# Performance work log

Hardware: AMD Instinct MI355X
Metric: run time of the kernel (lower is better)

The kernel has to match this reference:

```python
import jax, jax.numpy as jnp
import numpy as np

E, MAX_M, K, N = 8, 2048, 2048, 8192

def setup_inputs() -> dict:
    key = jax.random.key(0)
    k1, k2, k3 = jax.random.split(key, 3)
    x_padded = jax.random.normal(k1, (E, MAX_M, K), dtype=jnp.float32)
    stacked_weights = jax.random.normal(k2, (E, N, K), dtype=jnp.float32) * 0.02
    m_sizes = jax.random.randint(k3, (E,), 0, MAX_M, dtype=jnp.int32)
    return {"x_padded": x_padded, "stacked_weights": stacked_weights, "m_sizes": m_sizes}

def reference(x_padded, stacked_weights, m_sizes):
    # valid-token mask per expert: [E, MAX_M]
    mask = (jnp.arange(MAX_M, dtype=jnp.int32)[None, :] < m_sizes[:, None])
    # zero padded rows (pad_expert_inputs fills with zeros)
    x = jnp.where(mask[:, :, None], x_padded, jnp.zeros((), x_padded.dtype))
    # grouped GEMM via batched matmul: [E, M, K] x [E, N, K]^T -> [E, M, N]
    out = jnp.einsum('emk,enk->emn', x, stacked_weights)
    # rows beyond m_sizes[i] are sliced away in the original; mask them to zero
    return jnp.where(mask[:, :, None], out, jnp.zeros((), out.dtype))
```

## Files before the change

kernel.cpp:

```cpp
#include <hip/hip_runtime.h>
#include <hip/hip_bf16.h>


#define NE   8
#define MAXM 2048
#define KD   2048
#define ND   8192

#define BM   256
#define BN   256
#define BK   64
#define NT   (KD/BK)
#define TMB  (MAXM/BM)
#define TNB  (ND/BN)

typedef __attribute__((ext_vector_type(8))) short          short8;
typedef __attribute__((ext_vector_type(8))) unsigned short us8;
typedef __attribute__((ext_vector_type(4))) float          f32x4;
typedef __attribute__((ext_vector_type(4))) unsigned short us4;

__device__ __forceinline__ unsigned short f2bf(float f) {
    union { float f; unsigned u; } v; v.f = f;
    unsigned u = v.u;
    return (unsigned short)((u + 0x7FFFu + ((u >> 16) & 1u)) >> 16);
}

__device__ __forceinline__ void gload16(const void* g, void* l) {
    __builtin_amdgcn_global_load_lds(
        (const __attribute__((address_space(1))) void*)g,
        (__attribute__((address_space(3))) void*)l, 16, 0, 0);
}

__global__ __launch_bounds__(256) void cvt_kernel(const float* __restrict__ src,
                                                  unsigned short* __restrict__ dst,
                                                  int n8) {
    int i = blockIdx.x * blockDim.x + threadIdx.x;
    int stride = gridDim.x * blockDim.x;
    for (; i < n8; i += stride) {
        const f32x4* s = (const f32x4*)(src + (size_t)i * 8);
        f32x4 a = s[0], b = s[1];
        us8 v = (us8){f2bf(a[0]), f2bf(a[1]), f2bf(a[2]), f2bf(a[3]),
                      f2bf(b[0]), f2bf(b[1]), f2bf(b[2]), f2bf(b[3])};
        *(us8*)(dst + (size_t)i * 8) = v;
    }
}

__global__ __launch_bounds__(512, 2) void ggemm_8ph(
    const unsigned short* __restrict__ xb,
    const unsigned short* __restrict__ wb,
    const int*   __restrict__ ms,
    float*       __restrict__ out)
{
    int orig = blockIdx.x;
    int xcd  = orig & 7;
    int idx  = orig >> 3;
    int e    = idx >> 5;
    int u    = idx & 31;
    int br   = u >> 2;
    int bc   = xcd * 4 + (u & 3);

    int m_size = ms[e];
    int row0 = br * BM, col0 = bc * BN;
    float* outE = out + (size_t)e * MAXM * ND;
    int tid = threadIdx.x;

    if (row0 >= m_size) {
        f32x4 z = (f32x4){0.f, 0.f, 0.f, 0.f};
        #pragma unroll
        for (int j = 0; j < 32; ++j) {
            int i2 = tid + j * 512;
            int rr = i2 >> 6, cc = (i2 & 63) << 2;
            *(f32x4*)(outE + (size_t)(row0 + rr) * ND + col0 + cc) = z;
        }
        return;
    }

    const unsigned short* xE = xb + ((size_t)e * MAXM + row0) * KD;
    const unsigned short* wE = wb + ((size_t)e * ND   + col0) * KD;

    __shared__ unsigned short Ak[2][2][BM * 32];
    __shared__ unsigned short Bk[2][2][BN * 32];

    int wid = tid >> 6, lane = tid & 63;
    int wr = wid >> 2, wc = wid & 3;
    int lr = lane & 15, kg = lane >> 4;
    int srow = lane >> 2;
    int ss   = (lane & 3) ^ ((lane >> 3) & 3);

    auto stageA = [&](int b, int kh, int kt) {
        #pragma unroll
        for (int j = 0; j < 2; ++j) {
            int blk = wid * 2 + j;
            const unsigned short* src =
                xE + (size_t)(blk * 16 + srow) * KD + kt * BK + kh * 32 + ss * 8;
            gload16(src, (char*)&Ak[b][kh][0] + blk * 1024);
        }
    };
    auto stageB = [&](int b, int kh, int kt) {
        #pragma unroll
        for (int j = 0; j < 2; ++j) {
            int blk = wid * 2 + j;
            const unsigned short* src =
                wE + (size_t)(blk * 16 + srow) * KD + kt * BK + kh * 32 + ss * 8;
            gload16(src, (char*)&Bk[b][kh][0] + blk * 1024);
        }
    };

    auto ldA = [&](short8* a, int b, int kh) {
        #pragma unroll
        for (int mf = 0; mf < 8; ++mf) {
            int row  = wr * 128 + mf * 16 + lr;
            int slot = kg ^ ((row >> 1) & 3);
            a[mf] = *(const short8*)&Ak[b][kh][row * 32 + slot * 8];
        }
    };
    auto ldB = [&](short8* bf, int b, int kh, int nh) {
        #pragma unroll
        for (int i = 0; i < 2; ++i) {
            int row  = wc * 64 + (nh * 2 + i) * 16 + lr;
            int slot = kg ^ ((row >> 1) & 3);
            bf[i] = *(const short8*)&Bk[b][kh][row * 32 + slot * 8];
        }
    };

    f32x4 acc[8][4];
    #pragma unroll
    for (int mf = 0; mf < 8; ++mf)
        #pragma unroll
        for (int nf = 0; nf < 4; ++nf)
            acc[mf][nf] = (f32x4){0.f, 0.f, 0.f, 0.f};

    stageA(0, 0, 0); stageB(0, 0, 0);
    stageA(0, 1, 0); stageB(0, 1, 0);
    stageA(1, 0, 1); stageB(1, 0, 1);
    asm volatile("s_waitcnt vmcnt(8)" ::: "memory");
    __builtin_amdgcn_s_barrier();

    auto tile = [&](int b, int t) {
        short8 a[8], bf[2];
        ldA(a, b, 0); ldB(bf, b, 0, 0);
        if (t + 1 < NT) stageA(b ^ 1, 1, t + 1);
        __builtin_amdgcn_s_barrier();
        __builtin_amdgcn_s_setprio(1);
        #pragma unroll
        for (int mf = 0; mf < 8; ++mf) {
            acc[mf][0] = __builtin_amdgcn_mfma_f32_16x16x32_bf16(a[mf], bf[0], acc[mf][0], 0, 0, 0);
            acc[mf][1] = __builtin_amdgcn_mfma_f32_16x16x32_bf16(a[mf], bf[1], acc[mf][1], 0, 0, 0);
        }
        __builtin_amdgcn_s_setprio(0);
        __builtin_amdgcn_s_barrier();
        ldB(bf, b, 0, 1);
        if (t + 1 < NT) stageB(b ^ 1, 1, t + 1);
        __builtin_amdgcn_s_barrier();
        __builtin_amdgcn_s_setprio(1);
        #pragma unroll
        for (int mf = 0; mf < 8; ++mf) {
            acc[mf][2] = __builtin_amdgcn_mfma_f32_16x16x32_bf16(a[mf], bf[0], acc[mf][2], 0, 0, 0);
            acc[mf][3] = __builtin_amdgcn_mfma_f32_16x16x32_bf16(a[mf], bf[1], acc[mf][3], 0, 0, 0);
        }
        __builtin_amdgcn_s_setprio(0);
        if (t + 1 < NT) { asm volatile("s_waitcnt vmcnt(8)" ::: "memory"); }
        else            { asm volatile("s_waitcnt vmcnt(0)" ::: "memory"); }
        __builtin_amdgcn_s_barrier();
        ldA(a, b, 1); ldB(bf, b, 1, 0);
        if (t + 2 < NT) stageA(b, 0, t + 2);
        __builtin_amdgcn_s_barrier();
        __builtin_amdgcn_s_setprio(1);
        #pragma unroll
        for (int mf = 0; mf < 8; ++mf) {
            acc[mf][0] = __builtin_amdgcn_mfma_f32_16x16x32_bf16(a[mf], bf[0], acc[mf][0], 0, 0, 0);
            acc[mf][1] = __builtin_amdgcn_mfma_f32_16x16x32_bf16(a[mf], bf[1], acc[mf][1], 0, 0, 0);
        }
        __builtin_amdgcn_s_setprio(0);
        __builtin_amdgcn_s_barrier();
        ldB(bf, b, 1, 1);
        if (t + 2 < NT) stageB(b, 0, t + 2);
        __builtin_amdgcn_s_barrier();
        __builtin_amdgcn_s_setprio(1);
        #pragma unroll
        for (int mf = 0; mf < 8; ++mf) {
            acc[mf][2] = __builtin_amdgcn_mfma_f32_16x16x32_bf16(a[mf], bf[0], acc[mf][2], 0, 0, 0);
            acc[mf][3] = __builtin_amdgcn_mfma_f32_16x16x32_bf16(a[mf], bf[1], acc[mf][3], 0, 0, 0);
        }
        __builtin_amdgcn_s_setprio(0);
        if (t + 2 < NT)      { asm volatile("s_waitcnt vmcnt(8)" ::: "memory"); }
        else if (t + 1 < NT) { asm volatile("s_waitcnt vmcnt(4)" ::: "memory"); }
        else                 { asm volatile("s_waitcnt vmcnt(0)" ::: "memory"); }
        __builtin_amdgcn_s_barrier();
    };

    #pragma unroll 1
    for (int t = 0; t < NT; t += 2) {
        tile(0, t);
        tile(1, t + 1);
    }

    #pragma unroll
    for (int mf = 0; mf < 8; ++mf) {
        int rbase = row0 + wr * 128 + mf * 16 + kg * 4;
        #pragma unroll
        for (int nf = 0; nf < 4; ++nf) {
            int gc = col0 + wc * 64 + nf * 16 + lr;
            #pragma unroll
            for (int j = 0; j < 4; ++j) {
                int gr = rbase + j;
                float v = (gr < m_size) ? acc[mf][nf][j] : 0.f;
                outE[(size_t)gr * ND + gc] = v;
            }
        }
    }
}

#define FBM 128
#define FBK 32
#define FTM (MAXM/FBM)
#define FTN (ND/FBM)
#define FNT (KD/FBK)
#define LSTR 40
__global__ __launch_bounds__(256, 2) void ggemm_fused(
    const float* __restrict__ x, const float* __restrict__ w,
    const int* __restrict__ ms, float* __restrict__ out)
{
    int nwg  = gridDim.x;
    int orig = blockIdx.x;
    int cpx  = nwg >> 3;
    int bid  = (orig & 7) * cpx + (orig >> 3);
    int e   = bid / (FTM * FTN);
    int rem = bid % (FTM * FTN);
    int br  = rem % FTM;
    int bc  = rem / FTM;
    int m_size = ms[e];
    int row0 = br * FBM, col0 = bc * FBM;
    float* outE = out + (size_t)e * MAXM * ND;
    int tid = threadIdx.x;

    if (row0 >= m_size) {
        f32x4 z = (f32x4){0.f, 0.f, 0.f, 0.f};
        #pragma unroll
        for (int j = 0; j < 16; ++j) {
            int i2 = tid + j * 256;
            int rr = i2 >> 5, cc = (i2 & 31) << 2;
            *(f32x4*)(outE + (size_t)(row0 + rr) * ND + col0 + cc) = z;
        }
        return;
    }

    const float* xE = x + ((size_t)e * MAXM + row0) * KD;
    const float* wE = w + ((size_t)e * ND   + col0) * KD;

    __shared__ unsigned short As[2][FBM][LSTR];
    __shared__ unsigned short Bs[2][FBM][LSTR];

    int sr  = tid >> 3;
    int sc4 = tid & 7;
    int wid = tid >> 6, lane = tid & 63;
    int wr = wid >> 1, wc = wid & 1;
    int lr = lane & 15, kg = lane >> 4;

    f32x4 acc[4][4];
    #pragma unroll
    for (int m = 0; m < 4; ++m)
        #pragma unroll
        for (int n = 0; n < 4; ++n)
            acc[m][n] = (f32x4){0.f, 0.f, 0.f, 0.f};

    {
        #pragma unroll
        for (int j = 0; j < 4; ++j) {
            int r0 = sr + j * 32;
            f32x4 av = *(const f32x4*)(xE + (size_t)r0 * KD + sc4 * 4);
            f32x4 bv = *(const f32x4*)(wE + (size_t)r0 * KD + sc4 * 4);
            us4 ah = (us4){f2bf(av[0]), f2bf(av[1]), f2bf(av[2]), f2bf(av[3])};
            us4 bh = (us4){f2bf(bv[0]), f2bf(bv[1]), f2bf(bv[2]), f2bf(bv[3])};
            *(us4*)&As[0][r0][sc4 * 4] = ah;
            *(us4*)&Bs[0][r0][sc4 * 4] = bh;
        }
    }
    __syncthreads();

    for (int t = 0; t < FNT; ++t) {
        int cur = t & 1;
        f32x4 av[4], bv[4];
        bool pre = (t + 1 < FNT);
        if (pre) {
            const float* xk = xE + (size_t)(t + 1) * FBK;
            const float* wk = wE + (size_t)(t + 1) * FBK;
            #pragma unroll
            for (int j = 0; j < 4; ++j) {
                int r0 = sr + j * 32;
                av[j] = *(const f32x4*)(xk + (size_t)r0 * KD + sc4 * 4);
                bv[j] = *(const f32x4*)(wk + (size_t)r0 * KD + sc4 * 4);
            }
        }
        short8 a[4], b[4];
        #pragma unroll
        for (int m = 0; m < 4; ++m)
            a[m] = *(const short8*)&As[cur][wr * 64 + m * 16 + lr][kg * 8];
        #pragma unroll
        for (int n = 0; n < 4; ++n)
            b[n] = *(const short8*)&Bs[cur][wc * 64 + n * 16 + lr][kg * 8];
        #pragma unroll
        for (int m = 0; m < 4; ++m)
            #pragma unroll
            for (int n = 0; n < 4; ++n)
                acc[m][n] = __builtin_amdgcn_mfma_f32_16x16x32_bf16(a[m], b[n], acc[m][n], 0, 0, 0);

        if (pre) {
            int nb = cur ^ 1;
            #pragma unroll
            for (int j = 0; j < 4; ++j) {
                int r0 = sr + j * 32;
                us4 ah = (us4){f2bf(av[j][0]), f2bf(av[j][1]), f2bf(av[j][2]), f2bf(av[j][3])};
                us4 bh = (us4){f2bf(bv[j][0]), f2bf(bv[j][1]), f2bf(bv[j][2]), f2bf(bv[j][3])};
                *(us4*)&As[nb][r0][sc4 * 4] = ah;
                *(us4*)&Bs[nb][r0][sc4 * 4] = bh;
            }
        }
        __syncthreads();
    }

    #pragma unroll
    for (int m = 0; m < 4; ++m) {
        int rbase = row0 + wr * 64 + m * 16 + kg * 4;
        #pragma unroll
        for (int n = 0; n < 4; ++n) {
            int gc = col0 + wc * 64 + n * 16 + lr;
            #pragma unroll
            for (int j = 0; j < 4; ++j) {
                int gr = rbase + j;
                float v = (gr < m_size) ? acc[m][n][j] : 0.f;
                outE[(size_t)gr * ND + gc] = v;
            }
        }
    }
}

extern "C" void kernel_launch(void* const* d_in, const int* in_sizes, int n_in,
                              void* d_out, int out_size, void* d_ws, size_t ws_size,
                              hipStream_t stream) {
    const float* x  = (const float*)d_in[0];
    const float* w  = (const float*)d_in[1];
    const int*   ms = (const int*)d_in[2];
    float* out = (float*)d_out;

    const size_t xElems = (size_t)NE * MAXM * KD;
    const size_t wElems = (size_t)NE * ND   * KD;
    const size_t need   = (xElems + wElems) * 2;

    if (ws_size >= need) {
        unsigned short* xb = (unsigned short*)d_ws;
        unsigned short* wb = xb + xElems;
        cvt_kernel<<<2048, 256, 0, stream>>>(x, xb, (int)(xElems / 8));
        cvt_kernel<<<2048, 256, 0, stream>>>(w, wb, (int)(wElems / 8));
        ggemm_8ph<<<dim3(NE * TMB * TNB), dim3(512), 0, stream>>>(xb, wb, ms, out);
    } else {
        ggemm_fused<<<dim3(NE * (MAXM/FBM) * (ND/FBM)), dim3(256), 0, stream>>>(x, w, ms, out);
    }
}
```

Measured before the change: 600.3 us.

## Make grouped GEMM persistent over live tiles and convert only valid x rows

Replaces the one-tile-per-block grid with 256 persistent blocks. Each block owns one column tile and walks a rotated list of live (expert, row-block) tiles, prefetching the next tile's K slices across the tile boundary so the pipeline does not drain between tiles. The x conversion kernel now skips padded rows beyond m_sizes, which cuts conversion bandwidth. This trades the hardware scheduler's dynamic balancing for a fixed static schedule, and adds per-wave alive predication around the MFMA phases.

```diff
diff --git a/kernel.cpp b/kernel.cpp
--- a/kernel.cpp
+++ b/kernel.cpp
@@ -10,9 +10,7 @@
 #define BM   256
 #define BN   256
 #define BK   64
-#define NT   (KD/BK)
-#define TMB  (MAXM/BM)
-#define TNB  (ND/BN)
+#define NTS  (KD/BK)
 
 typedef __attribute__((ext_vector_type(8))) short          short8;
 typedef __attribute__((ext_vector_type(8))) unsigned short us8;
@@ -45,41 +43,69 @@
     }
 }
 
-__global__ __launch_bounds__(512, 2) void ggemm_8ph(
+__global__ __launch_bounds__(256) void cvt_x_kernel(const float* __restrict__ src,
+                                                    unsigned short* __restrict__ dst,
+                                                    const int* __restrict__ ms) {
+    int bid = blockIdx.x;
+    int e = bid >> 11, m = bid & 2047;
+    if (m >= ms[e]) return;
+    const float* s = src + ((size_t)e * MAXM + m) * KD;
+    unsigned short* d = dst + ((size_t)e * MAXM + m) * KD;
+    int t = threadIdx.x;
+    const f32x4* s4 = (const f32x4*)(s + t * 8);
+    f32x4 a = s4[0], b = s4[1];
+    us8 v = (us8){f2bf(a[0]), f2bf(a[1]), f2bf(a[2]), f2bf(a[3]),
+                  f2bf(b[0]), f2bf(b[1]), f2bf(b[2]), f2bf(b[3])};
+    *(us8*)(d + t * 8) = v;
+}
+
+__global__ __launch_bounds__(512, 2) void ggemm_pers(
     const unsigned short* __restrict__ xb,
     const unsigned short* __restrict__ wb,
     const int*   __restrict__ ms,
     float*       __restrict__ out)
 {
-    int orig = blockIdx.x;
-    int xcd  = orig & 7;
-    int idx  = orig >> 3;
-    int e    = idx >> 5;
-    int u    = idx & 31;
-    int br   = u >> 2;
-    int bc   = xcd * 4 + (u & 3);
-
-    int m_size = ms[e];
-    int row0 = br * BM, col0 = bc * BN;
-    float* outE = out + (size_t)e * MAXM * ND;
-    int tid = threadIdx.x;
-
-    if (row0 >= m_size) {
-        f32x4 z = (f32x4){0.f, 0.f, 0.f, 0.f};
-        #pragma unroll
-        for (int j = 0; j < 32; ++j) {
-            int i2 = tid + j * 512;
-            int rr = i2 >> 6, cc = (i2 & 63) << 2;
-            *(f32x4*)(outE + (size_t)(row0 + rr) * ND + col0 + cc) = z;
-        }
-        return;
-    }
-
-    const unsigned short* xE = xb + ((size_t)e * MAXM + row0) * KD;
-    const unsigned short* wE = wb + ((size_t)e * ND   + col0) * KD;
-
+    int p    = blockIdx.x;
+    int xcd  = p & 7;
+    int q    = p >> 3;
+    int rrot = q >> 2;
+    int bc   = xcd * 4 + (q & 3);
+    int col0 = bc * BN;
+    int tid  = threadIdx.x;
+
+    __shared__ int s_live[8];
+    __shared__ int s_nlive;
     __shared__ unsigned short Ak[2][2][BM * 32];
     __shared__ unsigned short Bk[2][2][BN * 32];
+
+    if (tid == 0) {
+        int n = 0;
+        #pragma unroll
+        for (int e = 0; e < NE; ++e) {
+            int br = (rrot + e) & 7;
+            if (br * BM < ms[e]) { s_live[n] = (e << 3) | br; ++n; }
+        }
+        s_nlive = n;
+    }
+
+    #pragma unroll 1
+    for (int e = 0; e < NE; ++e) {
+        int br   = (rrot + e) & 7;
+        int row0 = br * BM;
+        if (row0 >= ms[e]) {
+            float* outE = out + (size_t)e * MAXM * ND;
+            f32x4 z = (f32x4){0.f, 0.f, 0.f, 0.f};
+            #pragma unroll
+            for (int j = 0; j < 32; ++j) {
+                int i2 = tid + j * 512;
+                int rr = i2 >> 6, cc = (i2 & 63) << 2;
+                *(f32x4*)(outE + (size_t)(row0 + rr) * ND + col0 + cc) = z;
+            }
+        }
+    }
+    __syncthreads();
+    int nlive = s_nlive;
+    if (nlive == 0) return;
 
     int wid = tid >> 6, lane = tid & 63;
     int wr = wid >> 2, wc = wid & 3;
@@ -87,25 +113,24 @@
     int srow = lane >> 2;
     int ss   = (lane & 3) ^ ((lane >> 3) & 3);
 
-    auto stageA = [&](int b, int kh, int kt) {
+    auto stageA = [&](int b, int kh, const unsigned short* xP, int kt) {
         #pragma unroll
         for (int j = 0; j < 2; ++j) {
             int blk = wid * 2 + j;
             const unsigned short* src =
-                xE + (size_t)(blk * 16 + srow) * KD + kt * BK + kh * 32 + ss * 8;
+                xP + (size_t)(blk * 16 + srow) * KD + kt * BK + kh * 32 + ss * 8;
             gload16(src, (char*)&Ak[b][kh][0] + blk * 1024);
         }
     };
-    auto stageB = [&](int b, int kh, int kt) {
+    auto stageB = [&](int b, int kh, const unsigned short* wP, int kt) {
         #pragma unroll
         for (int j = 0; j < 2; ++j) {
             int blk = wid * 2 + j;
             const unsigned short* src =
-                wE + (size_t)(blk * 16 + srow) * KD + kt * BK + kh * 32 + ss * 8;
+                wP + (size_t)(blk * 16 + srow) * KD + kt * BK + kh * 32 + ss * 8;
             gload16(src, (char*)&Bk[b][kh][0] + blk * 1024);
         }
     };
-
     auto ldA = [&](short8* a, int b, int kh) {
         #pragma unroll
         for (int mf = 0; mf < 8; ++mf) {
@@ -130,83 +155,134 @@
         for (int nf = 0; nf < 4; ++nf)
             acc[mf][nf] = (f32x4){0.f, 0.f, 0.f, 0.f};
 
-    stageA(0, 0, 0); stageB(0, 0, 0);
-    stageA(0, 1, 0); stageB(0, 1, 0);
-    stageA(1, 0, 1); stageB(1, 0, 1);
+    const unsigned short *xC, *wC, *xN, *wN;
+    float *oC, *oN;
+    int msC, r0C, msN, r0N;
+    {
+        int v = s_live[0]; int e = v >> 3, br = v & 7;
+        r0C = br * BM; msC = ms[e];
+        xC = xb + ((size_t)e * MAXM + r0C) * KD;
+        wC = wb + ((size_t)e * ND + col0) * KD;
+        oC = out + (size_t)e * MAXM * ND;
+    }
+    if (nlive > 1) {
+        int v = s_live[1]; int e = v >> 3, br = v & 7;
+        r0N = br * BM; msN = ms[e];
+        xN = xb + ((size_t)e * MAXM + r0N) * KD;
+        wN = wb + ((size_t)e * ND + col0) * KD;
+        oN = out + (size_t)e * MAXM * ND;
+    } else { xN = xC; wN = wC; oN = oC; msN = msC; r0N = r0C; }
+
+    stageA(0, 0, xC, 0); stageB(0, 0, wC, 0);
+    stageA(0, 1, xC, 0); stageB(0, 1, wC, 0);
+    stageA(1, 0, xC, 1); stageB(1, 0, wC, 1);
     asm volatile("s_waitcnt vmcnt(8)" ::: "memory");
     __builtin_amdgcn_s_barrier();
 
-    auto tile = [&](int b, int t) {
-        short8 a[8], bf[2];
-        ldA(a, b, 0); ldB(bf, b, 0, 0);
-        if (t + 1 < NT) stageA(b ^ 1, 1, t + 1);
-        __builtin_amdgcn_s_barrier();
-        __builtin_amdgcn_s_setprio(1);
+    #pragma unroll 1
+    for (int s = 0; s < nlive; ++s) {
+        bool last  = (s + 1 >= nlive);
+        bool alive = (r0C + wr * 128) < msC;
+
+        auto tile = [&](int b, int kt) {
+            bool g1 = (kt + 1 < NTS) || (!last);
+            bool g2 = (kt + 2 < NTS) || (!last);
+            const unsigned short* xS1 = (kt + 1 < NTS) ? xC : xN;
+            const unsigned short* wS1 = (kt + 1 < NTS) ? wC : wN;
+            int k1 = (kt + 1 < NTS) ? kt + 1 : 0;
+            const unsigned short* xS2 = (kt + 2 < NTS) ? xC : xN;
+            const unsigned short* wS2 = (kt + 2 < NTS) ? wC : wN;
+            int k2 = (kt + 2 < NTS) ? kt + 2 : kt + 2 - NTS;
+
+            short8 a[8], bf[2];
+            if (alive) { ldA(a, b, 0); ldB(bf, b, 0, 0); }
+            if (g1) stageA(b ^ 1, 1, xS1, k1);
+            __builtin_amdgcn_s_barrier();
+            __builtin_amdgcn_s_setprio(1);
+            if (alive) {
+                #pragma unroll
+                for (int mf = 0; mf < 8; ++mf) {
+                    acc[mf][0] = __builtin_amdgcn_mfma_f32_16x16x32_bf16(a[mf], bf[0], acc[mf][0], 0, 0, 0);
+                    acc[mf][1] = __builtin_amdgcn_mfma_f32_16x16x32_bf16(a[mf], bf[1], acc[mf][1], 0, 0, 0);
+                }
+            }
+            __builtin_amdgcn_s_setprio(0);
+            __builtin_amdgcn_s_barrier();
+            if (alive) ldB(bf, b, 0, 1);
+            if (g1) stageB(b ^ 1, 1, wS1, k1);
+            __builtin_amdgcn_s_barrier();
+            __builtin_amdgcn_s_setprio(1);
+            if (alive) {
+                #pragma unroll
+                for (int mf = 0; mf < 8; ++mf) {
+                    acc[mf][2] = __builtin_amdgcn_mfma_f32_16x16x32_bf16(a[mf], bf[0], acc[mf][2], 0, 0, 0);
+                    acc[mf][3] = __builtin_amdgcn_mfma_f32_16x16x32_bf16(a[mf], bf[1], acc[mf][3], 0, 0, 0);
+                }
+            }
+            __builtin_amdgcn_s_setprio(0);
+            if (g1) { asm volatile("s_waitcnt vmcnt(8)" ::: "memory"); }
+            else    { asm volatile("s_waitcnt vmcnt(0)" ::: "memory"); }
+            __builtin_amdgcn_s_barrier();
+            if (alive) { ldA(a, b, 1); ldB(bf, b, 1, 0); }
+            if (g2) stageA(b, 0, xS2, k2);
+            __builtin_amdgcn_s_barrier();
+            __builtin_amdgcn_s_setprio(1);
+            if (alive) {
+                #pragma unroll
+                for (int mf = 0; mf < 8; ++mf) {
+                    acc[mf][0] = __builtin_amdgcn_mfma_f32_16x16x32_bf16(a[mf], bf[0], acc[mf][0], 0, 0, 0);
+                    acc[mf][1] = __builtin_amdgcn_mfma_f32_16x16x32_bf16(a[mf], bf[1], acc[mf][1], 0, 0, 0);
+                }
+            }
+            __builtin_amdgcn_s_setprio(0);
+            __builtin_amdgcn_s_barrier();
+            if (alive) ldB(bf, b, 1, 1);
+            if (g2) stageB(b, 0, wS2, k2);
+            __builtin_amdgcn_s_barrier();
+            __builtin_amdgcn_s_setprio(1);
+            if (alive) {
+                #pragma unroll
+                for (int mf = 0; mf < 8; ++mf) {
+                    acc[mf][2] = __builtin_amdgcn_mfma_f32_16x16x32_bf16(a[mf], bf[0], acc[mf][2], 0, 0, 0);
+                    acc[mf][3] = __builtin_amdgcn_mfma_f32_16x16x32_bf16(a[mf], bf[1], acc[mf][3], 0, 0, 0);
+                }
+            }
+            __builtin_amdgcn_s_setprio(0);
+            if (g2)      { asm volatile("s_waitcnt vmcnt(8)" ::: "memory"); }
+            else if (g1) { asm volatile("s_waitcnt vmcnt(4)" ::: "memory"); }
+            else         { asm volatile("s_waitcnt vmcnt(0)" ::: "memory"); }
+            __builtin_amdgcn_s_barrier();
+        };
+
+        #pragma unroll 1
+        for (int kt = 0; kt < NTS; kt += 2) {
+            tile(0, kt);
+            tile(1, kt + 1);
+        }
+
         #pragma unroll
         for (int mf = 0; mf < 8; ++mf) {
-            acc[mf][0] = __builtin_amdgcn_mfma_f32_16x16x32_bf16(a[mf], bf[0], acc[mf][0], 0, 0, 0);
-            acc[mf][1] = __builtin_amdgcn_mfma_f32_16x16x32_bf16(a[mf], bf[1], acc[mf][1], 0, 0, 0);
-        }
-        __builtin_amdgcn_s_setprio(0);
-        __builtin_amdgcn_s_barrier();
-        ldB(bf, b, 0, 1);
-        if (t + 1 < NT) stageB(b ^ 1, 1, t + 1);
-        __builtin_amdgcn_s_barrier();
-        __builtin_amdgcn_s_setprio(1);
-        #pragma unroll
-        for (int mf = 0; mf < 8; ++mf) {
-            acc[mf][2] = __builtin_amdgcn_mfma_f32_16x16x32_bf16(a[mf], bf[0], acc[mf][2], 0, 0, 0);
-            acc[mf][3] = __builtin_amdgcn_mfma_f32_16x16x32_bf16(a[mf], bf[1], acc[mf][3], 0, 0, 0);
-        }
-        __builtin_amdgcn_s_setprio(0);
-        if (t + 1 < NT) { asm volatile("s_waitcnt vmcnt(8)" ::: "memory"); }
-        else            { asm volatile("s_waitcnt vmcnt(0)" ::: "memory"); }
-        __builtin_amdgcn_s_barrier();
-        ldA(a, b, 1); ldB(bf, b, 1, 0);
-        if (t + 2 < NT) stageA(b, 0, t + 2);
-        __builtin_amdgcn_s_barrier();
-        __builtin_amdgcn_s_setprio(1);
-        #pragma unroll
-        for (int mf = 0; mf < 8; ++mf) {
-            acc[mf][0] = __builtin_amdgcn_mfma_f32_16x16x32_bf16(a[mf], bf[0], acc[mf][0], 0, 0, 0);
-            acc[mf][1] = __builtin_amdgcn_mfma_f32_16x16x32_bf16(a[mf], bf[1], acc[mf][1], 0, 0, 0);
-        }
-        __builtin_amdgcn_s_setprio(0);
-        __builtin_amdgcn_s_barrier();
-        ldB(bf, b, 1, 1);
-        if (t + 2 < NT) stageB(b, 0, t + 2);
-        __builtin_amdgcn_s_barrier();
-        __builtin_amdgcn_s_setprio(1);
-        #pragma unroll
-        for (int mf = 0; mf < 8; ++mf) {
-            acc[mf][2] = __builtin_amdgcn_mfma_f32_16x16x32_bf16(a[mf], bf[0], acc[mf][2], 0, 0, 0);
-            acc[mf][3] = __builtin_amdgcn_mfma_f32_16x16x32_bf16(a[mf], bf[1], acc[mf][3], 0, 0, 0);
-        }
-        __builtin_amdgcn_s_setprio(0);
-        if (t + 2 < NT)      { asm volatile("s_waitcnt vmcnt(8)" ::: "memory"); }
-        else if (t + 1 < NT) { asm volatile("s_waitcnt vmcnt(4)" ::: "memory"); }
-        else                 { asm volatile("s_waitcnt vmcnt(0)" ::: "memory"); }
-        __builtin_amdgcn_s_barrier();
-    };
-
-    #pragma unroll 1
-    for (int t = 0; t < NT; t += 2) {
-        tile(0, t);
-        tile(1, t + 1);
-    }
-
-    #pragma unroll
-    for (int mf = 0; mf < 8; ++mf) {
-        int rbase = row0 + wr * 128 + mf * 16 + kg * 4;
-        #pragma unroll
-        for (int nf = 0; nf < 4; ++nf) {
-            int gc = col0 + wc * 64 + nf * 16 + lr;
-            #pragma unroll
-            for (int j = 0; j < 4; ++j) {
-                int gr = rbase + j;
-                float v = (gr < m_size) ? acc[mf][nf][j] : 0.f;
-                outE[(size_t)gr * ND + gc] = v;
-            }
+            int rbase = r0C + wr * 128 + mf * 16 + kg * 4;
+            #pragma unroll
+            for (int nf = 0; nf < 4; ++nf) {
+                int gc = col0 + wc * 64 + nf * 16 + lr;
+                #pragma unroll
+                for (int j = 0; j < 4; ++j) {
+                    int gr = rbase + j;
+                    float v = (gr < msC) ? acc[mf][nf][j] : 0.f;
+                    oC[(size_t)gr * ND + gc] = v;
+                    acc[mf][nf][j] = 0.f;
+                }
+            }
+        }
+
+        xC = xN; wC = wN; oC = oN; msC = msN; r0C = r0N;
+        if (s + 2 < nlive) {
+            int v = s_live[s + 2]; int e = v >> 3, br = v & 7;
+            r0N = br * BM; msN = ms[e];
+            xN = xb + ((size_t)e * MAXM + r0N) * KD;
+            wN = wb + ((size_t)e * ND + col0) * KD;
+            oN = out + (size_t)e * MAXM * ND;
         }
     }
 }
@@ -350,9 +426,9 @@
     if (ws_size >= need) {
         unsigned short* xb = (unsigned short*)d_ws;
         unsigned short* wb = xb + xElems;
-        cvt_kernel<<<2048, 256, 0, stream>>>(x, xb, (int)(xElems / 8));
+        cvt_x_kernel<<<NE * MAXM, 256, 0, stream>>>(x, xb, ms);
         cvt_kernel<<<2048, 256, 0, stream>>>(w, wb, (int)(wElems / 8));
-        ggemm_8ph<<<dim3(NE * TMB * TNB), dim3(512), 0, stream>>>(xb, wb, ms, out);
+        ggemm_pers<<<256, 512, 0, stream>>>(xb, wb, ms, out);
     } else {
         ggemm_fused<<<dim3(NE * (MAXM/FBM) * (ND/FBM)), dim3(256), 0, stream>>>(x, w, ms, out);
     }
```

Result: faster. 583.9 us (-2.7%).
